# Performance work log

Measured on AMD Instinct MI355X. Metric: run time of the kernel, lower is better.

## Reference

```python
import jax, jax.numpy as jnp
import numpy as np

B, D, K, C = 32, 128, 512, 10  # batch, input dim, inner dim, clusters (all hardcoded in source)


def setup_inputs() -> dict:
    key = jax.random.key(0)
    k1, k2, k3, k4 = jax.random.split(key, 4)
    x_batch = jax.random.normal(k1, (B, D), dtype=jnp.float32)
    mu_c = jax.random.normal(k2, (C, D), dtype=jnp.float32)
    # parameters: torch.rand -> uniform [0,1)
    U = jax.random.uniform(k3, (D, K), dtype=jnp.float32)
    V = jax.random.uniform(k4, (D, K), dtype=jnp.float32)
    return {"x_batch": x_batch, "mu_c": mu_c, "U": U, "V": V}


def reference(x_batch, mu_c, U, V):
    # Original loops over batch: h_i = (mu_c @ V) @ (x_i @ U), then log_softmax over
    # the length-10 vector (dim=0 per sample). Batched equivalent:
    fac1 = x_batch @ U          # [B, K]
    fac2 = mu_c @ V             # [C, K]
    h = fac1 @ fac2.T           # [B, C]
    return jax.nn.log_softmax(h, axis=-1)
```

## Files before the change

### kernel.cpp

```cpp
#include <hip/hip_runtime.h>
#include <hip/hip_bf16.h>
#include <math.h>

#define BB 32
#define DD 128
#define KK 512
#define CC 10
#define KSPLIT 4
#define KCH (KK / KSPLIT)

__global__ __launch_bounds__(KCH) void fac_kernel(
    const float* __restrict__ x, const float* __restrict__ mu,
    const float* __restrict__ U, const float* __restrict__ V,
    float* __restrict__ fac)
{
    const int r  = blockIdx.x;
    const int ks = blockIdx.y;
    const int k  = ks * KCH + threadIdx.x;

    const float* __restrict__ row = (r < BB) ? (x + r * DD) : (mu + (r - BB) * DD);
    const float* __restrict__ W   = (r < BB) ? U : V;

    float acc = 0.0f;
    #pragma unroll 16
    for (int d = 0; d < DD; ++d) {
        acc = fmaf(row[d], W[d * KK + k], acc);
    }
    fac[r * KK + k] = acc;
}

__global__ __launch_bounds__(64) void h_softmax_kernel(
    const float* __restrict__ fac, float* __restrict__ out)
{
    const int b    = blockIdx.x;
    const int lane = threadIdx.x;

    const float* __restrict__ f1 = fac + b * KK;
    const float* __restrict__ f2 = fac + BB * KK;

    const float4* f1v = (const float4*)(f1 + lane * 8);
    const float4 p0 = f1v[0];
    const float4 p1 = f1v[1];

    float hrow[CC];
    #pragma unroll
    for (int c = 0; c < CC; ++c) {
        const float4* f2v = (const float4*)(f2 + c * KK + lane * 8);
        const float4 q0 = f2v[0];
        const float4 q1 = f2v[1];
        float s = p0.x * q0.x + p0.y * q0.y + p0.z * q0.z + p0.w * q0.w
                + p1.x * q1.x + p1.y * q1.y + p1.z * q1.z + p1.w * q1.w;
        #pragma unroll
        for (int off = 32; off > 0; off >>= 1) {
            s += __shfl_xor(s, off);
        }
        hrow[c] = s;
    }

    float mx = hrow[0];
    #pragma unroll
    for (int c = 1; c < CC; ++c) mx = fmaxf(mx, hrow[c]);
    float sum = 0.0f;
    #pragma unroll
    for (int c = 0; c < CC; ++c) sum += __expf(hrow[c] - mx);
    const float lse = mx + __logf(sum);

    if (lane < CC) {
        float v = hrow[0];
        #pragma unroll
        for (int c = 1; c < CC; ++c) v = (lane == c) ? hrow[c] : v;
        out[b * CC + lane] = v - lse;
    }
}

extern "C" void kernel_launch(void* const* d_in, const int* in_sizes, int n_in,
                              void* d_out, int out_size, void* d_ws, size_t ws_size,
                              hipStream_t stream)
{
    const float* x  = (const float*)d_in[0];
    const float* mu = (const float*)d_in[1];
    const float* U  = (const float*)d_in[2];
    const float* V  = (const float*)d_in[3];
    float* out = (float*)d_out;
    float* fac = (float*)d_ws;

    dim3 gridA(BB + CC, KSPLIT);
    fac_kernel<<<gridA, KCH, 0, stream>>>(x, mu, U, V, fac);
    h_softmax_kernel<<<BB, 64, 0, stream>>>(fac, out);
}
```

Baseline: 65.42 us.

## Fuse factor GEMVs, inner product and log-softmax into one kernel

Replaces the two-kernel pipeline (factor computation into workspace, then dot products plus log-softmax) with a single kernel of one block per batch row. Each block recomputes x_b@U and the full mu@V for its row, reduces through shuffles and shared memory, then applies log-softmax. This removes a kernel launch and the workspace round trip, but repeats the mu@V work in all 32 blocks, and 32 blocks only partly fill the GPU.

Result: slower. 74.80 us (+14.3%).

```diff
diff --git a/kernel.cpp b/kernel.cpp
--- a/kernel.cpp
+++ b/kernel.cpp
@@ -6,70 +6,69 @@
 #define DD 128
 #define KK 512
 #define CC 10
-#define KSPLIT 4
-#define KCH (KK / KSPLIT)
 
-__global__ __launch_bounds__(KCH) void fac_kernel(
+__global__ __launch_bounds__(KK, 1) void fused_kernel(
     const float* __restrict__ x, const float* __restrict__ mu,
     const float* __restrict__ U, const float* __restrict__ V,
-    float* __restrict__ fac)
-{
-    const int r  = blockIdx.x;
-    const int ks = blockIdx.y;
-    const int k  = ks * KCH + threadIdx.x;
-
-    const float* __restrict__ row = (r < BB) ? (x + r * DD) : (mu + (r - BB) * DD);
-    const float* __restrict__ W   = (r < BB) ? U : V;
-
-    float acc = 0.0f;
-    #pragma unroll 16
-    for (int d = 0; d < DD; ++d) {
-        acc = fmaf(row[d], W[d * KK + k], acc);
-    }
-    fac[r * KK + k] = acc;
-}
-
-__global__ __launch_bounds__(64) void h_softmax_kernel(
-    const float* __restrict__ fac, float* __restrict__ out)
+    float* __restrict__ out)
 {
     const int b    = blockIdx.x;
-    const int lane = threadIdx.x;
+    const int t    = threadIdx.x;
+    const int lane = t & 63;
+    const int wave = t >> 6;
 
-    const float* __restrict__ f1 = fac + b * KK;
-    const float* __restrict__ f2 = fac + BB * KK;
+    __shared__ float part[8][CC + 1];
 
-    const float4* f1v = (const float4*)(f1 + lane * 8);
-    const float4 p0 = f1v[0];
-    const float4 p1 = f1v[1];
+    const float* __restrict__ xb = x + b * DD;
 
-    float hrow[CC];
+    float f1 = 0.0f;
+    float acc[CC];
+    #pragma unroll
+    for (int c = 0; c < CC; ++c) acc[c] = 0.0f;
+
+    #pragma unroll 4
+    for (int d = 0; d < DD; ++d) {
+        const float u = U[d * KK + t];
+        const float v = V[d * KK + t];
+        f1 = fmaf(xb[d], u, f1);
+        #pragma unroll
+        for (int c = 0; c < CC; ++c)
+            acc[c] = fmaf(mu[c * DD + d], v, acc[c]);
+    }
+
     #pragma unroll
     for (int c = 0; c < CC; ++c) {
-        const float4* f2v = (const float4*)(f2 + c * KK + lane * 8);
-        const float4 q0 = f2v[0];
-        const float4 q1 = f2v[1];
-        float s = p0.x * q0.x + p0.y * q0.y + p0.z * q0.z + p0.w * q0.w
-                + p1.x * q1.x + p1.y * q1.y + p1.z * q1.z + p1.w * q1.w;
+        float s = f1 * acc[c];
         #pragma unroll
-        for (int off = 32; off > 0; off >>= 1) {
+        for (int off = 32; off > 0; off >>= 1)
             s += __shfl_xor(s, off);
+        if (lane == 0) part[wave][c] = s;
+    }
+    __syncthreads();
+
+    if (wave == 0) {
+        float h[CC];
+        #pragma unroll
+        for (int c = 0; c < CC; ++c) {
+            float s = 0.0f;
+            #pragma unroll
+            for (int w = 0; w < 8; ++w) s += part[w][c];
+            h[c] = s;
         }
-        hrow[c] = s;
-    }
+        float mx = h[0];
+        #pragma unroll
+        for (int c = 1; c < CC; ++c) mx = fmaxf(mx, h[c]);
+        float sum = 0.0f;
+        #pragma unroll
+        for (int c = 0; c < CC; ++c) sum += __expf(h[c] - mx);
+        const float lse = mx + __logf(sum);
 
-    float mx = hrow[0];
-    #pragma unroll
-    for (int c = 1; c < CC; ++c) mx = fmaxf(mx, hrow[c]);
-    float sum = 0.0f;
-    #pragma unroll
-    for (int c = 0; c < CC; ++c) sum += __expf(hrow[c] - mx);
-    const float lse = mx + __logf(sum);
-
-    if (lane < CC) {
-        float v = hrow[0];
-        #pragma unroll
-        for (int c = 1; c < CC; ++c) v = (lane == c) ? hrow[c] : v;
-        out[b * CC + lane] = v - lse;
+        if (lane < CC) {
+            float v = h[0];
+            #pragma unroll
+            for (int c = 1; c < CC; ++c) v = (lane == c) ? h[c] : v;
+            out[b * CC + lane] = v - lse;
+        }
     }
 }
 
@@ -82,9 +81,7 @@
     const float* U  = (const float*)d_in[2];
     const float* V  = (const float*)d_in[3];
     float* out = (float*)d_out;
-    float* fac = (float*)d_ws;
+    (void)d_ws; (void)ws_size;
 
-    dim3 gridA(BB + CC, KSPLIT);
-    fac_kernel<<<gridA, KCH, 0, stream>>>(x, mu, U, V, fac);
-    h_softmax_kernel<<<BB, 64, 0, stream>>>(fac, out);
+    fused_kernel<<<BB, KK, 0, stream>>>(x, mu, U, V, out);
 }
```
